# Kernel optimization log

Measured on AMD Instinct MI355X. Metric: run time of the kernel, lower is better.

Reference implementation:

```python
import jax, jax.numpy as jnp
import numpy as np

LAMBDA = 0.95   # fast-weight decay
ETA = 0.5       # Hebbian write rate
EPS = 1e-5      # LayerNorm epsilon
S_LOOP = 2      # inner read steps


def setup_inputs() -> dict:
    key = jax.random.key(0)
    ks = jax.random.split(key, 3)
    T, B, d_g, d_h = 32, 32, 256, 512
    z_seq = jax.random.normal(ks[0], (T, B, d_g), dtype=jnp.float32)
    # kaiming-uniform-ish / xavier-ish scaled weights
    W_h = jax.random.normal(ks[1], (d_h, d_h), dtype=jnp.float32) * (2.0 / d_h) ** 0.5
    W_g = jax.random.normal(ks[2], (d_h, d_g), dtype=jnp.float32) * (2.0 / (d_h + d_g)) ** 0.5
    b_h = jnp.zeros((d_h,), jnp.float32)
    ln_gamma = jnp.ones((d_h,), jnp.float32)
    ln_beta = jnp.zeros((d_h,), jnp.float32)
    return {"z_seq": z_seq, "W_h": W_h, "W_g": W_g, "b_h": b_h,
            "ln_gamma": ln_gamma, "ln_beta": ln_beta}


def reference(z_seq, W_h, W_g, b_h, ln_gamma, ln_beta):
    T, B, _ = z_seq.shape
    d_h = W_h.shape[0]

    def ln(x):
        mu = jnp.mean(x, axis=-1, keepdims=True)
        var = jnp.mean((x - mu) ** 2, axis=-1, keepdims=True)
        return (x - mu) * jax.lax.rsqrt(var + EPS) * ln_gamma + ln_beta

    def inner_read(h_base, A):
        # h = relu(LN(h_base)); then S fast-weight reads h <- relu(LN(h_base + A h))
        h = jax.nn.relu(ln(h_base))
        for _ in range(S_LOOP):
            Ah = jnp.einsum('bij,bj->bi', A, h)  # [B, d_h]
            h = jax.nn.relu(ln(h_base + Ah))
        return h

    def step(carry, z_t):
        h, A = carry
        h_base = h @ W_h.T + z_t @ W_g.T + b_h  # [B, d_h]
        h = inner_read(h_base, A)
        # Hebbian outer-product write: A <- lambda*A + eta * h h^T
        A = LAMBDA * A + ETA * jnp.einsum('bi,bj->bij', h, h)
        return (h, A), None

    h0 = jnp.zeros((B, d_h), z_seq.dtype)
    A0 = jnp.zeros((B, d_h, d_h), z_seq.dtype)
    (h, A), _ = jax.lax.scan(step, (h0, A0), z_seq[:-1])

    # last step: read-only (no A update)
    h_base = h @ W_h.T + z_seq[-1] @ W_g.T + b_h
    h = inner_read(h_base, A)
    return h
```

## Files before the change

kernel.cpp:

```cpp
#include <hip/hip_runtime.h>

typedef __attribute__((ext_vector_type(8))) short short8;
typedef __attribute__((ext_vector_type(4))) float f32x4;

constexpr int T_STEPS = 32;
constexpr int BATCH   = 32;
constexpr int DG      = 256;
constexpr int DH      = 512;
constexpr int NHIST   = 31;
constexpr int LDH     = 528;
constexpr int LDT     = 40;
constexpr float LAMBDA_ = 0.95f;
constexpr float ETA_    = 0.5f;
constexpr float EPS_    = 1e-5f;

__device__ __forceinline__ uint bf16cvt(float f) {
  uint u = __float_as_uint(f);
  return (u + 0x7FFFu + ((u >> 16) & 1u)) >> 16;
}
__device__ __forceinline__ uint pack2(float a, float b) {
  return bf16cvt(a) | (bf16cvt(b) << 16);
}
__device__ __forceinline__ float bf2f(ushort u) {
  return __uint_as_float(((uint)u) << 16);
}

__global__ __launch_bounds__(512) void pack_kernel(
    const float* __restrict__ Wh, uint4* __restrict__ Wp) {
  const int f  = blockIdx.x * 512 + threadIdx.x;
  const int lf = f & 63;
  const int kk = (f >> 6) & 15;
  const int mt = f >> 10;
  const int r  = mt * 16 + (lf & 15);
  const int k0 = kk * 32 + (lf >> 4) * 8;
  const float4 a = *reinterpret_cast<const float4*>(Wh + (size_t)r * DH + k0);
  const float4 b = *reinterpret_cast<const float4*>(Wh + (size_t)r * DH + k0 + 4);
  Wp[f] = make_uint4(pack2(a.x, a.y), pack2(a.z, a.w),
                     pack2(b.x, b.y), pack2(b.z, b.w));
}

__global__ __launch_bounds__(512, 2) void rnn_kernel(
    const uint4* __restrict__ Wp, const float* __restrict__ z,
    const float* __restrict__ Wg, const float* __restrict__ bh,
    const float* __restrict__ g, const float* __restrict__ be,
    float* __restrict__ out) {
  __shared__ uint4  Wres[2 * 32 * 64];
  __shared__ ushort area_bf[T_STEPS][LDH];
  __shared__ ushort histT[DH][LDT];
  __shared__ float  part[DH];
  __shared__ float  h_s[DH];
  __shared__ ushort hbf[DH];
  __shared__ float  red1[8], red2[8];
  __shared__ float  cc[NHIST + 1];
  __shared__ float  lam_pow[NHIST];

  const int tid  = threadIdx.x;
  const int lane = tid & 63;
  const int wave = tid >> 6;
  const int c    = lane & 15;
  const int gq   = lane >> 4;
  const int b    = blockIdx.x;
  const int r    = tid;

  if (tid == 0) {
    float p = 1.f;
    for (int k = 0; k < NHIST; ++k) { lam_pow[k] = p; p *= LAMBDA_; }
  }
  if (tid < NHIST + 1) cc[tid] = 0.f;
  {
    uint4 zz = make_uint4(0u, 0u, 0u, 0u);
#pragma unroll
    for (int i = 0; i < 5; ++i)
      reinterpret_cast<uint4*>(&histT[r][0])[i] = zz;
  }
#pragma unroll
  for (int i2 = 0; i2 < 8; ++i2) {
    const int i  = i2 * 512 + tid;
    const int mt = i >> 7, kkl = (i >> 6) & 1, ln2 = i & 63;
    Wres[i] = Wp[(size_t)(mt * 16 + kkl) * 64 + ln2];
  }

#pragma unroll
  for (int mt4 = 0; mt4 < 4; ++mt4) {
    const int mt = wave * 4 + mt4;
    f32x4 acc0 = {0.f,0.f,0.f,0.f}, acc1 = {0.f,0.f,0.f,0.f};
#pragma unroll
    for (int kk = 0; kk < 8; ++kk) {
      const int k0 = kk * 32 + gq * 8;
      const float4 a  = *reinterpret_cast<const float4*>(Wg + (size_t)(mt*16 + c) * DG + k0);
      const float4 a2 = *reinterpret_cast<const float4*>(Wg + (size_t)(mt*16 + c) * DG + k0 + 4);
      const uint4 afu = make_uint4(pack2(a.x,a.y), pack2(a.z,a.w),
                                   pack2(a2.x,a2.y), pack2(a2.z,a2.w));
      const float* zb0 = z + ((size_t)c        * BATCH + b) * DG + k0;
      const float* zb1 = z + ((size_t)(16 + c) * BATCH + b) * DG + k0;
      const float4 b00 = *reinterpret_cast<const float4*>(zb0);
      const float4 b01 = *reinterpret_cast<const float4*>(zb0 + 4);
      const float4 b10 = *reinterpret_cast<const float4*>(zb1);
      const float4 b11 = *reinterpret_cast<const float4*>(zb1 + 4);
      const uint4 bf0 = make_uint4(pack2(b00.x,b00.y), pack2(b00.z,b00.w),
                                   pack2(b01.x,b01.y), pack2(b01.z,b01.w));
      const uint4 bf1 = make_uint4(pack2(b10.x,b10.y), pack2(b10.z,b10.w),
                                   pack2(b11.x,b11.y), pack2(b11.z,b11.w));
      acc0 = __builtin_amdgcn_mfma_f32_16x16x32_bf16(
          __builtin_bit_cast(short8, afu), __builtin_bit_cast(short8, bf0), acc0, 0,0,0);
      acc1 = __builtin_amdgcn_mfma_f32_16x16x32_bf16(
          __builtin_bit_cast(short8, afu), __builtin_bit_cast(short8, bf1), acc1, 0,0,0);
    }
    *reinterpret_cast<uint2*>(&area_bf[c][mt*16 + gq*4]) =
        make_uint2(pack2(acc0.x, acc0.y), pack2(acc0.z, acc0.w));
    *reinterpret_cast<uint2*>(&area_bf[16 + c][mt*16 + gq*4]) =
        make_uint2(pack2(acc1.x, acc1.y), pack2(acc1.z, acc1.w));
  }
  __syncthreads();

  const float bh_r = bh[r], g_r = g[r], be_r = be[r];

  auto ln = [&](float x) -> float {
    float s1 = x, s2 = x * x;
#pragma unroll
    for (int off = 32; off; off >>= 1) {
      s1 += __shfl_xor(s1, off, 64);
      s2 += __shfl_xor(s2, off, 64);
    }
    if (lane == 0) { red1[wave] = s1; red2[wave] = s2; }
    __syncthreads();
    float a = 0.f, q = 0.f;
#pragma unroll
    for (int w2 = 0; w2 < 8; ++w2) { a += red1[w2]; q += red2[w2]; }
    const float mu = a * (1.f / DH);
    const float rs = rsqrtf(q * (1.f / DH) - mu * mu + EPS_);
    const float hv2 = fmaxf((x - mu) * rs * g_r + be_r, 0.f);
    h_s[r] = hv2;
    hbf[r] = (ushort)bf16cvt(hv2);
    __syncthreads();
    return hv2;
  };

  float hv = 0.f;
  for (int t = 0; t < T_STEPS; ++t) {
    float xb;
    if (t == 0) {
      xb = bf2f(area_bf[0][r]) + bh_r;
    } else {
      f32x4 acc[4] = {{0.f,0.f,0.f,0.f},{0.f,0.f,0.f,0.f},
                      {0.f,0.f,0.f,0.f},{0.f,0.f,0.f,0.f}};
      uint4 bfr[8];
#pragma unroll
      for (int kk = 0; kk < 8; ++kk)
        bfr[kk] = *reinterpret_cast<const uint4*>(&hbf[kk*32 + gq*8]);
#pragma unroll
      for (int kk = 0; kk < 2; ++kk) {
        const short8 bv = __builtin_bit_cast(short8, bfr[kk]);
#pragma unroll
        for (int mt4 = 0; mt4 < 4; ++mt4) {
          const uint4 au = Wres[(size_t)((wave*4 + mt4)*2 + kk) * 64 + lane];
          acc[mt4] = __builtin_amdgcn_mfma_f32_16x16x32_bf16(
              __builtin_bit_cast(short8, au), bv, acc[mt4], 0,0,0);
        }
      }
#pragma unroll
      for (int kk = 2; kk < 8; ++kk) {
        const short8 bv = __builtin_bit_cast(short8, bfr[kk]);
#pragma unroll
        for (int mt4 = 0; mt4 < 4; ++mt4) {
          const uint4 au = Wp[(size_t)((wave*4 + mt4)*16 + kk) * 64 + lane];
          acc[mt4] = __builtin_amdgcn_mfma_f32_16x16x32_bf16(
              __builtin_bit_cast(short8, au), bv, acc[mt4], 0,0,0);
        }
      }
#pragma unroll
      for (int kk = 0; kk < 8; ++kk)
        bfr[kk] = *reinterpret_cast<const uint4*>(&hbf[(kk + 8)*32 + gq*8]);
#pragma unroll
      for (int kk = 8; kk < 16; ++kk) {
        const short8 bv = __builtin_bit_cast(short8, bfr[kk - 8]);
#pragma unroll
        for (int mt4 = 0; mt4 < 4; ++mt4) {
          const uint4 au = Wp[(size_t)((wave*4 + mt4)*16 + kk) * 64 + lane];
          acc[mt4] = __builtin_amdgcn_mfma_f32_16x16x32_bf16(
              __builtin_bit_cast(short8, au), bv, acc[mt4], 0,0,0);
        }
      }
      if (c == 0) {
#pragma unroll
        for (int mt4 = 0; mt4 < 4; ++mt4)
          *reinterpret_cast<f32x4*>(&part[(wave*4 + mt4)*16 + gq*4]) = acc[mt4];
      }
      __syncthreads();
      xb = part[r] + bf2f(area_bf[t][r]) + bh_r;
    }

    hv = ln(xb);

    if (t > 0) {
      for (int s = 0; s < 2; ++s) {
        const float4 c0 = *reinterpret_cast<const float4*>(&h_s[lane * 8]);
        const float4 c1 = *reinterpret_cast<const float4*>(&h_s[lane * 8 + 4]);
        for (int sp = wave; sp < t; sp += 8) {
          const uint4 hw = *reinterpret_cast<const uint4*>(&area_bf[sp][lane * 8]);
          float d;
          d =      __uint_as_float(hw.x << 16)          * c0.x;
          d = fmaf(__uint_as_float(hw.x & 0xFFFF0000u), c0.y, d);
          d = fmaf(__uint_as_float(hw.y << 16),         c0.z, d);
          d = fmaf(__uint_as_float(hw.y & 0xFFFF0000u), c0.w, d);
          d = fmaf(__uint_as_float(hw.z << 16),         c1.x, d);
          d = fmaf(__uint_as_float(hw.z & 0xFFFF0000u), c1.y, d);
          d = fmaf(__uint_as_float(hw.w << 16),         c1.z, d);
          d = fmaf(__uint_as_float(hw.w & 0xFFFF0000u), c1.w, d);
#pragma unroll
          for (int off = 32; off; off >>= 1) d += __shfl_xor(d, off, 64);
          if (lane == 0) cc[sp] = ETA_ * lam_pow[t - 1 - sp] * d;
        }
        __syncthreads();
        float ah = 0.f;
#pragma unroll
        for (int q8 = 0; q8 < 4; ++q8) {
          const uint4 hw = *reinterpret_cast<const uint4*>(&histT[r][q8 * 8]);
          const uint w0 = hw.x, w1 = hw.y, w2 = hw.z, w3 = hw.w;
          ah = fmaf(cc[q8*8+0], __uint_as_float(w0 << 16),          ah);
          ah = fmaf(cc[q8*8+1], __uint_as_float(w0 & 0xFFFF0000u),  ah);
          ah = fmaf(cc[q8*8+2], __uint_as_float(w1 << 16),          ah);
          ah = fmaf(cc[q8*8+3], __uint_as_float(w1 & 0xFFFF0000u),  ah);
          ah = fmaf(cc[q8*8+4], __uint_as_float(w2 << 16),          ah);
          ah = fmaf(cc[q8*8+5], __uint_as_float(w2 & 0xFFFF0000u),  ah);
          ah = fmaf(cc[q8*8+6], __uint_as_float(w3 << 16),          ah);
          ah = fmaf(cc[q8*8+7], __uint_as_float(w3 & 0xFFFF0000u),  ah);
        }
        hv = ln(xb + ah);
      }
    }

    if (t < T_STEPS - 1) {
      const ushort h16 = (ushort)bf16cvt(hv);
      area_bf[t][r] = h16;
      histT[r][t]   = h16;
    }
  }

  out[(size_t)b * DH + r] = hv;
}

extern "C" void kernel_launch(void* const* d_in, const int* in_sizes, int n_in,
                              void* d_out, int out_size, void* d_ws, size_t ws_size,
                              hipStream_t stream) {
  const float* z     = (const float*)d_in[0];
  const float* W_h   = (const float*)d_in[1];
  const float* W_g   = (const float*)d_in[2];
  const float* b_h   = (const float*)d_in[3];
  const float* gamma = (const float*)d_in[4];
  const float* beta  = (const float*)d_in[5];
  float* out = (float*)d_out;

  uint4* Wp = (uint4*)d_ws;

  pack_kernel<<<dim3(64), dim3(512), 0, stream>>>(W_h, Wp);
  rnn_kernel<<<dim3(BATCH), dim3(512), 0, stream>>>(Wp, z, W_g, b_h,
                                                    gamma, beta, out);
}
```

Baseline: 280.9 us.

## Drop transposed history buffer and use freed LDS to keep more W_h resident

Removes the transposed history copy histT and computes the A·h reconstruction by reading area_bf column-wise with a variable-length loop over past steps. The freed shared memory holds a third k-slice of the packed recurrent weight (RKK=3), so fewer MFMA A-operands are fetched from global/L2 each step. The trade-off is a scalar per-step loop of ushort LDS reads in place of vectorised reads of a fixed 32-entry row, plus a larger LDS footprint for weights.

```diff
diff --git a/kernel.cpp b/kernel.cpp
--- a/kernel.cpp
+++ b/kernel.cpp
@@ -9,7 +9,7 @@
 constexpr int DH      = 512;
 constexpr int NHIST   = 31;
 constexpr int LDH     = 528;
-constexpr int LDT     = 40;
+constexpr int RKK     = 3;
 constexpr float LAMBDA_ = 0.95f;
 constexpr float ETA_    = 0.5f;
 constexpr float EPS_    = 1e-5f;
@@ -44,9 +44,8 @@
     const float* __restrict__ Wg, const float* __restrict__ bh,
     const float* __restrict__ g, const float* __restrict__ be,
     float* __restrict__ out) {
-  __shared__ uint4  Wres[2 * 32 * 64];
+  __shared__ uint4  Wres[RKK * 32 * 64];
   __shared__ ushort area_bf[T_STEPS][LDH];
-  __shared__ ushort histT[DH][LDT];
   __shared__ float  part[DH];
   __shared__ float  h_s[DH];
   __shared__ ushort hbf[DH];
@@ -67,17 +66,16 @@
     for (int k = 0; k < NHIST; ++k) { lam_pow[k] = p; p *= LAMBDA_; }
   }
   if (tid < NHIST + 1) cc[tid] = 0.f;
-  {
-    uint4 zz = make_uint4(0u, 0u, 0u, 0u);
-#pragma unroll
-    for (int i = 0; i < 5; ++i)
-      reinterpret_cast<uint4*>(&histT[r][0])[i] = zz;
-  }
-#pragma unroll
-  for (int i2 = 0; i2 < 8; ++i2) {
-    const int i  = i2 * 512 + tid;
-    const int mt = i >> 7, kkl = (i >> 6) & 1, ln2 = i & 63;
-    Wres[i] = Wp[(size_t)(mt * 16 + kkl) * 64 + ln2];
+
+#pragma unroll
+  for (int kkl = 0; kkl < RKK; ++kkl) {
+#pragma unroll
+    for (int i2 = 0; i2 < 4; ++i2) {
+      const int f2  = i2 * 512 + tid;
+      const int mt  = f2 >> 6;
+      const int ln2 = f2 & 63;
+      Wres[(mt * RKK + kkl) * 64 + ln2] = Wp[(size_t)(mt * 16 + kkl) * 64 + ln2];
+    }
   }
 
 #pragma unroll
@@ -149,17 +147,17 @@
       for (int kk = 0; kk < 8; ++kk)
         bfr[kk] = *reinterpret_cast<const uint4*>(&hbf[kk*32 + gq*8]);
 #pragma unroll
-      for (int kk = 0; kk < 2; ++kk) {
+      for (int kk = 0; kk < RKK; ++kk) {
         const short8 bv = __builtin_bit_cast(short8, bfr[kk]);
 #pragma unroll
         for (int mt4 = 0; mt4 < 4; ++mt4) {
-          const uint4 au = Wres[(size_t)((wave*4 + mt4)*2 + kk) * 64 + lane];
+          const uint4 au = Wres[((wave*4 + mt4)*RKK + kk) * 64 + lane];
           acc[mt4] = __builtin_amdgcn_mfma_f32_16x16x32_bf16(
               __builtin_bit_cast(short8, au), bv, acc[mt4], 0,0,0);
         }
       }
 #pragma unroll
-      for (int kk = 2; kk < 8; ++kk) {
+      for (int kk = RKK; kk < 8; ++kk) {
         const short8 bv = __builtin_bit_cast(short8, bfr[kk]);
 #pragma unroll
         for (int mt4 = 0; mt4 < 4; ++mt4) {
@@ -213,28 +211,13 @@
         }
         __syncthreads();
         float ah = 0.f;
-#pragma unroll
-        for (int q8 = 0; q8 < 4; ++q8) {
-          const uint4 hw = *reinterpret_cast<const uint4*>(&histT[r][q8 * 8]);
-          const uint w0 = hw.x, w1 = hw.y, w2 = hw.z, w3 = hw.w;
-          ah = fmaf(cc[q8*8+0], __uint_as_float(w0 << 16),          ah);
-          ah = fmaf(cc[q8*8+1], __uint_as_float(w0 & 0xFFFF0000u),  ah);
-          ah = fmaf(cc[q8*8+2], __uint_as_float(w1 << 16),          ah);
-          ah = fmaf(cc[q8*8+3], __uint_as_float(w1 & 0xFFFF0000u),  ah);
-          ah = fmaf(cc[q8*8+4], __uint_as_float(w2 << 16),          ah);
-          ah = fmaf(cc[q8*8+5], __uint_as_float(w2 & 0xFFFF0000u),  ah);
-          ah = fmaf(cc[q8*8+6], __uint_as_float(w3 << 16),          ah);
-          ah = fmaf(cc[q8*8+7], __uint_as_float(w3 & 0xFFFF0000u),  ah);
-        }
+        for (int sp = 0; sp < t; ++sp)
+          ah = fmaf(cc[sp], bf2f(area_bf[sp][r]), ah);
         hv = ln(xb + ah);
       }
     }
 
-    if (t < T_STEPS - 1) {
-      const ushort h16 = (ushort)bf16cvt(hv);
-      area_bf[t][r] = h16;
-      histT[r][t]   = h16;
-    }
+    if (t < T_STEPS - 1) area_bf[t][r] = (ushort)bf16cvt(hv);
   }
 
   out[(size_t)b * DH + r] = hv;
```

Result: slower. 306.0 us (+8.9%).
